# Performance work log

Measured on AMD Instinct MI355X. Metric: run time of the kernel, lower is better.

The kernel has to match this reference:

```python
import jax, jax.numpy as jnp
import numpy as np

B, L, H, N, DM = 16, 32768, 64, 16, 32


def setup_inputs() -> dict:
    key = jax.random.key(0)
    ks = jax.random.split(key, 16)
    inp = {}
    inp['x'] = jax.random.normal(ks[0], (B, L, H), dtype=jnp.float32)
    inp['control_parameters'] = jax.random.uniform(ks[1], (B, 2), dtype=jnp.float32)
    inp['W0'] = jax.random.normal(ks[2], (2, DM), dtype=jnp.float32) / np.sqrt(2.0)
    inp['b0'] = jnp.zeros((DM,), dtype=jnp.float32)
    inp['W1'] = jax.random.normal(ks[3], (DM, DM), dtype=jnp.float32) / np.sqrt(DM)
    inp['b1'] = jnp.zeros((DM,), dtype=jnp.float32)
    inp['W2'] = jax.random.normal(ks[4], (DM, DM), dtype=jnp.float32) / np.sqrt(DM)
    inp['b2'] = jnp.zeros((DM,), dtype=jnp.float32)
    # BlockV1 input linear
    inp['W_lin'] = jax.random.normal(ks[5], (H, H), dtype=jnp.float32) / np.sqrt(H)
    inp['b_lin'] = jnp.zeros((H,), dtype=jnp.float32)
    # DSSM / S4D parameters (S4D-Lin init)
    log_dt_min, log_dt_max = np.log(1e-3), np.log(1e-1)
    inp['log_dt'] = (log_dt_min + (log_dt_max - log_dt_min)
                     * jax.random.uniform(ks[6], (H,), dtype=jnp.float32))
    inp['A_re'] = -0.5 * jnp.ones((H, N), dtype=jnp.float32)
    inp['A_im'] = jnp.broadcast_to(np.pi * jnp.arange(N, dtype=jnp.float32), (H, N)).copy()
    inp['C_re'] = jax.random.normal(ks[7], (H, N), dtype=jnp.float32) / np.sqrt(2.0)
    inp['C_im'] = jax.random.normal(ks[8], (H, N), dtype=jnp.float32) / np.sqrt(2.0)
    inp['D'] = jax.random.normal(ks[9], (H,), dtype=jnp.float32)
    # FiLM: Linear(DM, 2*H) -> (gamma, beta)
    inp['W_film'] = jax.random.normal(ks[10], (DM, 2 * H), dtype=jnp.float32) / np.sqrt(DM)
    inp['b_film'] = jnp.zeros((2 * H,), dtype=jnp.float32)
    return inp


def _s4d_kernel(log_dt, A_re, A_im, C_re, C_im, length):
    # Diagonal SSM (S4D) convolution kernel via ZOH discretization.
    dt = jnp.exp(log_dt)[:, None]                      # [H,1]
    A = A_re + 1j * A_im                               # [H,N]
    dtA = dt * A                                       # [H,N]
    C = (C_re + 1j * C_im) * (jnp.exp(dtA) - 1.0) / A  # [H,N]
    t = jnp.arange(length, dtype=jnp.float32)          # [L]
    # Vandermonde: K[h,l] = 2 * Re( sum_n C[h,n] * exp(dtA[h,n])^l )
    vand = jnp.exp(dtA[:, :, None] * t)                # [H,N,L] complex
    return 2.0 * jnp.einsum('hn,hnl->hl', C, vand).real


def reference(x, control_parameters, W0, b0, W1, b1, W2, b2,
              W_lin, b_lin, log_dt, A_re, A_im, C_re, C_im, D,
              W_film, b_film):
    gelu = jax.nn.gelu
    # control-parameter MLP -> conditioning vector [B, DM]
    cond = gelu(control_parameters @ W0 + b0)
    cond = gelu(cond @ W1 + b1)
    cond = gelu(cond @ W2 + b2)
    # BlockV1: Linear + act
    h = gelu(x @ W_lin + b_lin)          # [B,L,H]
    u = jnp.swapaxes(h, 1, 2)            # [B,H,L]
    length = u.shape[-1]
    # S4D global convolution via FFT (linear, non-circular)
    K = _s4d_kernel(log_dt, A_re, A_im, C_re, C_im, length)   # [H,L]
    n = 2 * length
    Kf = jnp.fft.rfft(K, n=n)            # [H, n//2+1]
    uf = jnp.fft.rfft(u, n=n)            # [B,H, n//2+1]
    y = jnp.fft.irfft(uf * Kf, n=n)[..., :length] + D[:, None] * u  # [B,H,L]
    y = jnp.swapaxes(y, 1, 2)            # [B,L,H]
    # FiLM conditioning (no batch norm)
    gb = cond @ W_film + b_film          # [B, 2H]
    g, b = jnp.split(gb, 2, axis=-1)     # [B,H] each
    y = gelu(y * g[:, None, :] + b[:, None, :])
    # side-chain gate: elementwise multiply with input
    return x * y
```

## Files before the change

kernel.cpp:

```cpp
#include <hip/hip_runtime.h>
#include <hip/hip_bf16.h>
#include <math.h>

#define B_ 16
#define L_ 32768
#define H_ 64
#define N_ 16
#define DM_ 32
#define T_ 128
#define C_ 256
#define TS_ 16
#define US_ 68

typedef __attribute__((ext_vector_type(8))) short short8;
typedef __attribute__((ext_vector_type(4))) float floatx4;
typedef __attribute__((ext_vector_type(2))) float f32x2;

__device__ __forceinline__ float fast_gelu(float v) {
    float z = fmaf(0.044715f * v, v * v, v) * 0.7978845608028654f;
#if __has_builtin(__builtin_amdgcn_exp2f) && __has_builtin(__builtin_amdgcn_rcpf)
    float e = __builtin_amdgcn_exp2f(z * 2.8853900817779268f);
    float t = 1.0f - 2.0f * __builtin_amdgcn_rcpf(e + 1.0f);
#else
    float t = tanhf(z);
#endif
    return 0.5f * v * (1.0f + t);
}

__device__ __forceinline__ unsigned short bf16_rne(float f) {
    unsigned u = __float_as_uint(f);
    return (unsigned short)((u + 0x7FFFu + ((u >> 16) & 1u)) >> 16);
}
__device__ __forceinline__ float bf16_tof(unsigned short h) {
    return __uint_as_float(((unsigned)h) << 16);
}
__device__ __forceinline__ void cvt8(const float* f, short8* hi, short8* lo) {
    union { unsigned u[4]; short8 s; } Hh, Ll;
    #pragma unroll
    for (int jp = 0; jp < 4; ++jp) {
        unsigned short h0 = bf16_rne(f[2*jp]), h1 = bf16_rne(f[2*jp+1]);
        Hh.u[jp] = (unsigned)h0 | ((unsigned)h1 << 16);
        float l0 = f[2*jp]   - bf16_tof(h0);
        float l1 = f[2*jp+1] - bf16_tof(h1);
        Ll.u[jp] = (unsigned)bf16_rne(l0) | ((unsigned)bf16_rne(l1) << 16);
    }
    *hi = Hh.s; *lo = Ll.s;
}

__device__ __forceinline__ void pk_step(f32x2& s, f32x2 w, f32x2 uv0) {
    f32x2 t;
    asm("v_pk_fma_f32 %0, %1, %2, %3 op_sel:[1,1,0] op_sel_hi:[1,0,1] neg_lo:[1,0,0]"
        : "=v"(t) : "v"(w), "v"(s), "v"(uv0));
    asm("v_pk_fma_f32 %0, %1, %0, %2 op_sel_hi:[0,1,1]"
        : "+v"(s) : "v"(w), "v"(t));
}
__device__ __forceinline__ void pk_acc(f32x2& y, f32x2 c, f32x2 s) {
    asm("v_pk_fma_f32 %0, %1, %2, %0"
        : "+v"(y) : "v"(c), "v"(s));
}

__global__ void cond_film_kernel(const float* __restrict__ cp,
    const float* __restrict__ W0, const float* __restrict__ b0,
    const float* __restrict__ W1, const float* __restrict__ b1,
    const float* __restrict__ W2, const float* __restrict__ b2,
    const float* __restrict__ Wf, const float* __restrict__ bf,
    float* __restrict__ film) {
    __shared__ float ca[B_][DM_];
    __shared__ float cb[B_][DM_];
    int tid = threadIdx.x;
    int b = tid >> 5, j = tid & 31;
    float acc = fmaf(cp[b*2+0], W0[j], fmaf(cp[b*2+1], W0[DM_+j], b0[j]));
    ca[b][j] = fast_gelu(acc);
    __syncthreads();
    acc = b1[j];
    #pragma unroll
    for (int i = 0; i < DM_; ++i) acc = fmaf(ca[b][i], W1[i*DM_+j], acc);
    cb[b][j] = fast_gelu(acc);
    __syncthreads();
    acc = b2[j];
    #pragma unroll
    for (int i = 0; i < DM_; ++i) acc = fmaf(cb[b][i], W2[i*DM_+j], acc);
    float c2 = fast_gelu(acc);
    __syncthreads();
    ca[b][j] = c2;
    __syncthreads();
    #pragma unroll
    for (int t = 0; t < 4; ++t) {
        int k = j + DM_*t;
        float a = bf[k];
        #pragma unroll
        for (int i = 0; i < DM_; ++i) a = fmaf(ca[b][i], Wf[i*2*H_+k], a);
        film[b*2*H_ + k] = a;
    }
}

__global__ void coef_kernel(const float* __restrict__ log_dt,
    const float* __restrict__ A_re, const float* __restrict__ A_im,
    const float* __restrict__ C_re, const float* __restrict__ C_im,
    float* __restrict__ coef) {
    int g = blockIdx.x * blockDim.x + threadIdx.x;
    if (g >= H_*N_) return;
    int h = g >> 4, n = g & 15;
    float dt = expf(log_dt[h]);
    float Ar = A_re[h*N_+n], Ai = A_im[h*N_+n];
    float ar = dt*Ar, ai = dt*Ai;
    float er = expf(ar);
    float wr = er * cosf(ai), wi = er * sinf(ai);
    float eT = expf((float)T_ * ar);
    float aT = (float)T_ * ai;
    float wTr = eT * cosf(aT), wTi = eT * sinf(aT);
    float d  = Ar*Ar + Ai*Ai;
    float nr = wr - 1.0f, ni = wi;
    float qr = (nr*Ar + ni*Ai) / d;
    float qi = (ni*Ar - nr*Ai) / d;
    float Cr = C_re[h*N_+n], Ci = C_im[h*N_+n];
    float cr = 2.0f * (Cr*qr - Ci*qi);
    float ci = 2.0f * (Cr*qi + Ci*qr);
    coef[(n*6+0)*H_+h] = wr;
    coef[(n*6+1)*H_+h] = wi;
    coef[(n*6+2)*H_+h] = wTr;
    coef[(n*6+3)*H_+h] = wTi;
    coef[(n*6+4)*H_+h] = cr;
    coef[(n*6+5)*H_+h] = ci;
}

__global__ void chunk_scan_kernel(float* __restrict__ states,
                                  const float* __restrict__ coef) {
    int t = blockIdx.x * blockDim.x + threadIdx.x;
    int h = t & 63, n = (t >> 6) & 15, b = t >> 10;
    float wTr = coef[(n*6+2)*H_+h], wTi = coef[(n*6+3)*H_+h];
    float2* sp = (float2*)states + ((size_t)b*C_)*N_*H_ + (size_t)n*H_ + h;
    const int stride = N_*H_;
    float car = 0.f, cai = 0.f;
    float2 buf[8];
    #pragma unroll
    for (int i = 0; i < 8; ++i) buf[i] = sp[(size_t)i*stride];
    for (int cg = 0; cg < C_; cg += 8) {
        float2 nb[8];
        #pragma unroll
        for (int i = 0; i < 8; ++i)
            nb[i] = (cg + 8 + i < C_) ? sp[(size_t)(cg+8+i)*stride]
                                      : make_float2(0.f, 0.f);
        #pragma unroll
        for (int i = 0; i < 8; ++i) {
            float2 v = buf[i];
            sp[(size_t)(cg+i)*stride] = make_float2(car, cai);
            float nr2 = fmaf(wTr, car, fmaf(-wTi, cai, v.x));
            float ni2 = fmaf(wTr, cai, fmaf( wTi, car, v.y));
            car = nr2; cai = ni2;
            buf[i] = nb[i];
        }
    }
}

template<int PHASE>
__global__ __launch_bounds__(256, 3)
void gemm_scan_kernel(const float* __restrict__ x,
                      const float* __restrict__ W_lin, const float* __restrict__ b_lin,
                      const float* __restrict__ coef, float* __restrict__ states,
                      const float* __restrict__ D, const float* __restrict__ film,
                      float* __restrict__ out) {
    __shared__ __align__(16) unsigned short Wf[16*64*8];
    __shared__ float uld[4][TS_*US_];
    const int lane = threadIdx.x & 63;
    const int wv   = threadIdx.x >> 6;
    const int q    = blockIdx.x*4 + wv;
    const int b    = q >> 8;
    const int c    = q & 255;
    const int m    = lane & 15;
    const int quad = lane >> 4;

    for (int kt = 0; kt < 2; ++kt)
        for (int nt = 0; nt < 4; ++nt) {
            float f[8];
            #pragma unroll
            for (int j = 0; j < 8; ++j)
                f[j] = W_lin[(kt*32 + quad*8 + j)*H_ + nt*16 + m];
            short8 hi, lo;
            cvt8(f, &hi, &lo);
            ((short8*)Wf)[(kt*4 + nt)*64 + lane]     = hi;
            ((short8*)Wf)[((2+kt)*4 + nt)*64 + lane] = lo;
        }

    f32x2 w2[N_], s2[N_], c2[N_];
    float g_ = 0.f, be_ = 0.f, Dh = 0.f;
    #pragma unroll
    for (int n = 0; n < N_; ++n) {
        w2[n].x = coef[(n*6+0)*H_ + lane];
        w2[n].y = coef[(n*6+1)*H_ + lane];
    }
    if (PHASE == 1) {
        #pragma unroll
        for (int n = 0; n < N_; ++n) s2[n] = (f32x2){0.f, 0.f};
    } else {
        #pragma unroll
        for (int n = 0; n < N_; ++n) {
            c2[n].x = coef[(n*6+4)*H_ + lane];
            c2[n].y = coef[(n*6+5)*H_ + lane];
            size_t idx = (((size_t)q*N_ + n)*H_ + lane)*2;
            s2[n] = *(const f32x2*)(states + idx);
        }
        g_  = film[b*2*H_ + lane];
        be_ = film[b*2*H_ + H_ + lane];
        Dh  = D[lane];
    }
    float blv[4];
    #pragma unroll
    for (int nt = 0; nt < 4; ++nt) blv[nt] = b_lin[nt*16 + m];

    const float* xp = x + ((size_t)b*L_ + (size_t)c*T_)*H_;
    float* op = out + ((size_t)b*L_ + (size_t)c*T_)*H_;
    float* myu = uld[wv];

    for (int s = 0; s < T_/TS_; ++s) {
        const float* xs = xp + s*TS_*H_;
        short8 ah[2], al[2];
        #pragma unroll
        for (int kt = 0; kt < 2; ++kt) {
            const float* src = xs + m*H_ + kt*32 + quad*8;
            float4 v0 = *(const float4*)(src);
            float4 v1 = *(const float4*)(src + 4);
            float f[8] = {v0.x, v0.y, v0.z, v0.w, v1.x, v1.y, v1.z, v1.w};
            cvt8(f, &ah[kt], &al[kt]);
        }
        #pragma unroll
        for (int nt = 0; nt < 4; ++nt) {
            floatx4 acc = {0.f, 0.f, 0.f, 0.f};
            #pragma unroll
            for (int kt = 0; kt < 2; ++kt) {
                short8 bh = ((short8*)Wf)[(kt*4 + nt)*64 + lane];
                short8 bl = ((short8*)Wf)[((2+kt)*4 + nt)*64 + lane];
                acc = __builtin_amdgcn_mfma_f32_16x16x32_bf16(ah[kt], bh, acc, 0, 0, 0);
                acc = __builtin_amdgcn_mfma_f32_16x16x32_bf16(al[kt], bh, acc, 0, 0, 0);
                acc = __builtin_amdgcn_mfma_f32_16x16x32_bf16(ah[kt], bl, acc, 0, 0, 0);
            }
            #pragma unroll
            for (int r = 0; r < 4; ++r) {
                int row = quad*4 + r;
                float uv = fast_gelu(acc[r] + blv[nt]);
                myu[row*US_ + nt*16 + m] = uv;
            }
        }
        for (int l = 0; l < TS_; ++l) {
            float uv = myu[l*US_ + lane];
            f32x2 uv0 = {uv, 0.f};
            if (PHASE == 1) {
                #pragma unroll
                for (int n = 0; n < N_; ++n) pk_step(s2[n], w2[n], uv0);
            } else {
                float xg = xs[l*H_ + lane];
                f32x2 y2 = {0.f, 0.f};
                #pragma unroll
                for (int n = 0; n < N_; ++n) {
                    pk_step(s2[n], w2[n], uv0);
                    pk_acc(y2, c2[n], s2[n]);
                }
                float y  = fmaf(Dh, uv, y2.x - y2.y);
                float yg = fast_gelu(fmaf(y, g_, be_));
                op[(s*TS_ + l)*H_ + lane] = xg * yg;
            }
        }
    }
    if (PHASE == 1) {
        #pragma unroll
        for (int n = 0; n < N_; ++n) {
            size_t idx = (((size_t)q*N_ + n)*H_ + lane)*2;
            *(f32x2*)(states + idx) = s2[n];
        }
    }
}

extern "C" void kernel_launch(void* const* d_in, const int* in_sizes, int n_in,
                              void* d_out, int out_size, void* d_ws, size_t ws_size,
                              hipStream_t stream) {
    const float* x     = (const float*)d_in[0];
    const float* cp    = (const float*)d_in[1];
    const float* W0    = (const float*)d_in[2];
    const float* b0    = (const float*)d_in[3];
    const float* W1    = (const float*)d_in[4];
    const float* b1    = (const float*)d_in[5];
    const float* W2    = (const float*)d_in[6];
    const float* b2    = (const float*)d_in[7];
    const float* W_lin = (const float*)d_in[8];
    const float* b_lin = (const float*)d_in[9];
    const float* log_dt= (const float*)d_in[10];
    const float* A_re  = (const float*)d_in[11];
    const float* A_im  = (const float*)d_in[12];
    const float* C_re  = (const float*)d_in[13];
    const float* C_im  = (const float*)d_in[14];
    const float* D     = (const float*)d_in[15];
    const float* W_f   = (const float*)d_in[16];
    const float* b_f   = (const float*)d_in[17];
    float* out = (float*)d_out;

    float* film   = (float*)d_ws;
    float* coef   = film + B_*2*H_;
    float* states = coef + 6*H_*N_;

    cond_film_kernel<<<1, 512, 0, stream>>>(cp, W0, b0, W1, b1, W2, b2,
                                            W_f, b_f, film);
    coef_kernel<<<4, 256, 0, stream>>>(log_dt, A_re, A_im, C_re, C_im, coef);
    gemm_scan_kernel<1><<<(B_*C_)/4, 256, 0, stream>>>(x, W_lin, b_lin, coef,
                                                       states, nullptr, nullptr, nullptr);
    chunk_scan_kernel<<<(B_*N_*H_)/256, 256, 0, stream>>>(states, coef);
    gemm_scan_kernel<3><<<(B_*C_)/4, 256, 0, stream>>>(x, W_lin, b_lin, coef,
                                                       states, D, film, out);
}
```

Measured before the change: 502.6 us.

## Double chunk count to 512 and stage x tile in LDS for output phase

Halves the chunk length (128 to 64 steps) so twice as many wavefronts run the two scan phases, shortening each wave's serial recurrence. The chunk-scan and coef kernels are parameterized accordingly, with a fallback to the old 256-chunk config if the workspace is too small. In phase 3, the x tile is copied into shared memory while loading for the GEMM, so the gate multiply reads LDS instead of re-reading global memory. The per-step u and x values are also prefetched one step ahead. The trade-offs are a doubled state buffer, a longer sequential inter-chunk scan, and extra LDS usage that may lower occupancy.

```diff
diff --git a/kernel.cpp b/kernel.cpp
--- a/kernel.cpp
+++ b/kernel.cpp
@@ -7,8 +7,6 @@
 #define H_ 64
 #define N_ 16
 #define DM_ 32
-#define T_ 128
-#define C_ 256
 #define TS_ 16
 #define US_ 68
 
@@ -97,7 +95,7 @@
 __global__ void coef_kernel(const float* __restrict__ log_dt,
     const float* __restrict__ A_re, const float* __restrict__ A_im,
     const float* __restrict__ C_re, const float* __restrict__ C_im,
-    float* __restrict__ coef) {
+    float* __restrict__ coef, float Tf) {
     int g = blockIdx.x * blockDim.x + threadIdx.x;
     if (g >= H_*N_) return;
     int h = g >> 4, n = g & 15;
@@ -106,8 +104,8 @@
     float ar = dt*Ar, ai = dt*Ai;
     float er = expf(ar);
     float wr = er * cosf(ai), wi = er * sinf(ai);
-    float eT = expf((float)T_ * ar);
-    float aT = (float)T_ * ai;
+    float eT = expf(Tf * ar);
+    float aT = Tf * ai;
     float wTr = eT * cosf(aT), wTi = eT * sinf(aT);
     float d  = Ar*Ar + Ai*Ai;
     float nr = wr - 1.0f, ni = wi;
@@ -125,21 +123,21 @@
 }
 
 __global__ void chunk_scan_kernel(float* __restrict__ states,
-                                  const float* __restrict__ coef) {
+                                  const float* __restrict__ coef, int Cc) {
     int t = blockIdx.x * blockDim.x + threadIdx.x;
     int h = t & 63, n = (t >> 6) & 15, b = t >> 10;
     float wTr = coef[(n*6+2)*H_+h], wTi = coef[(n*6+3)*H_+h];
-    float2* sp = (float2*)states + ((size_t)b*C_)*N_*H_ + (size_t)n*H_ + h;
+    float2* sp = (float2*)states + ((size_t)b*Cc)*N_*H_ + (size_t)n*H_ + h;
     const int stride = N_*H_;
     float car = 0.f, cai = 0.f;
     float2 buf[8];
     #pragma unroll
     for (int i = 0; i < 8; ++i) buf[i] = sp[(size_t)i*stride];
-    for (int cg = 0; cg < C_; cg += 8) {
+    for (int cg = 0; cg < Cc; cg += 8) {
         float2 nb[8];
         #pragma unroll
         for (int i = 0; i < 8; ++i)
-            nb[i] = (cg + 8 + i < C_) ? sp[(size_t)(cg+8+i)*stride]
+            nb[i] = (cg + 8 + i < Cc) ? sp[(size_t)(cg+8+i)*stride]
                                       : make_float2(0.f, 0.f);
         #pragma unroll
         for (int i = 0; i < 8; ++i) {
@@ -153,20 +151,22 @@
     }
 }
 
-template<int PHASE>
+template<int PHASE, int CC>
 __global__ __launch_bounds__(256, 3)
 void gemm_scan_kernel(const float* __restrict__ x,
                       const float* __restrict__ W_lin, const float* __restrict__ b_lin,
                       const float* __restrict__ coef, float* __restrict__ states,
                       const float* __restrict__ D, const float* __restrict__ film,
                       float* __restrict__ out) {
+    constexpr int TT = L_/CC;
     __shared__ __align__(16) unsigned short Wf[16*64*8];
     __shared__ float uld[4][TS_*US_];
+    __shared__ float xld[(PHASE==3) ? 4*TS_*US_ : 4];
     const int lane = threadIdx.x & 63;
     const int wv   = threadIdx.x >> 6;
     const int q    = blockIdx.x*4 + wv;
-    const int b    = q >> 8;
-    const int c    = q & 255;
+    const int b    = q / CC;
+    const int c    = q % CC;
     const int m    = lane & 15;
     const int quad = lane >> 4;
 
@@ -208,11 +208,12 @@
     #pragma unroll
     for (int nt = 0; nt < 4; ++nt) blv[nt] = b_lin[nt*16 + m];
 
-    const float* xp = x + ((size_t)b*L_ + (size_t)c*T_)*H_;
-    float* op = out + ((size_t)b*L_ + (size_t)c*T_)*H_;
+    const float* xp = x + ((size_t)b*L_ + (size_t)c*TT)*H_;
+    float* op = out + ((size_t)b*L_ + (size_t)c*TT)*H_;
     float* myu = uld[wv];
-
-    for (int s = 0; s < T_/TS_; ++s) {
+    float* myx = (PHASE==3) ? &xld[wv*TS_*US_] : nullptr;
+
+    for (int s = 0; s < TT/TS_; ++s) {
         const float* xs = xp + s*TS_*H_;
         short8 ah[2], al[2];
         #pragma unroll
@@ -220,6 +221,11 @@
             const float* src = xs + m*H_ + kt*32 + quad*8;
             float4 v0 = *(const float4*)(src);
             float4 v1 = *(const float4*)(src + 4);
+            if (PHASE == 3) {
+                float* dst = &myx[m*US_ + kt*32 + quad*8];
+                *(float4*)(dst)     = v0;
+                *(float4*)(dst + 4) = v1;
+            }
             float f[8] = {v0.x, v0.y, v0.z, v0.w, v1.x, v1.y, v1.z, v1.w};
             cvt8(f, &ah[kt], &al[kt]);
         }
@@ -241,24 +247,28 @@
                 myu[row*US_ + nt*16 + m] = uv;
             }
         }
+        float uvc = myu[lane];
+        float xgc = (PHASE==3) ? myx[lane] : 0.f;
         for (int l = 0; l < TS_; ++l) {
-            float uv = myu[l*US_ + lane];
-            f32x2 uv0 = {uv, 0.f};
+            int ln = (l+1) & (TS_-1);
+            float uvn = myu[ln*US_ + lane];
+            float xgn = (PHASE==3) ? myx[ln*US_ + lane] : 0.f;
+            f32x2 uv0 = {uvc, 0.f};
             if (PHASE == 1) {
                 #pragma unroll
                 for (int n = 0; n < N_; ++n) pk_step(s2[n], w2[n], uv0);
             } else {
-                float xg = xs[l*H_ + lane];
                 f32x2 y2 = {0.f, 0.f};
                 #pragma unroll
                 for (int n = 0; n < N_; ++n) {
                     pk_step(s2[n], w2[n], uv0);
                     pk_acc(y2, c2[n], s2[n]);
                 }
-                float y  = fmaf(Dh, uv, y2.x - y2.y);
+                float y  = fmaf(Dh, uvc, y2.x - y2.y);
                 float yg = fast_gelu(fmaf(y, g_, be_));
-                op[(s*TS_ + l)*H_ + lane] = xg * yg;
+                op[(s*TS_ + l)*H_ + lane] = xgc * yg;
             }
+            uvc = uvn; xgc = xgn;
         }
     }
     if (PHASE == 1) {
@@ -299,10 +309,24 @@
 
     cond_film_kernel<<<1, 512, 0, stream>>>(cp, W0, b0, W1, b1, W2, b2,
                                             W_f, b_f, film);
-    coef_kernel<<<4, 256, 0, stream>>>(log_dt, A_re, A_im, C_re, C_im, coef);
-    gemm_scan_kernel<1><<<(B_*C_)/4, 256, 0, stream>>>(x, W_lin, b_lin, coef,
-                                                       states, nullptr, nullptr, nullptr);
-    chunk_scan_kernel<<<(B_*N_*H_)/256, 256, 0, stream>>>(states, coef);
-    gemm_scan_kernel<3><<<(B_*C_)/4, 256, 0, stream>>>(x, W_lin, b_lin, coef,
-                                                       states, D, film, out);
-}
+
+    size_t need64 = (size_t)(B_*2*H_ + 6*H_*N_)*4
+                  + (size_t)B_*512*N_*H_*2*4;
+    if (ws_size >= need64) {
+        coef_kernel<<<4, 256, 0, stream>>>(log_dt, A_re, A_im, C_re, C_im,
+                                           coef, 64.0f);
+        gemm_scan_kernel<1,512><<<(B_*512)/4, 256, 0, stream>>>(
+            x, W_lin, b_lin, coef, states, nullptr, nullptr, nullptr);
+        chunk_scan_kernel<<<(B_*N_*H_)/256, 256, 0, stream>>>(states, coef, 512);
+        gemm_scan_kernel<3,512><<<(B_*512)/4, 256, 0, stream>>>(
+            x, W_lin, b_lin, coef, states, D, film, out);
+    } else {
+        coef_kernel<<<4, 256, 0, stream>>>(log_dt, A_re, A_im, C_re, C_im,
+                                           coef, 128.0f);
+        gemm_scan_kernel<1,256><<<(B_*256)/4, 256, 0, stream>>>(
+            x, W_lin, b_lin, coef, states, nullptr, nullptr, nullptr);
+        chunk_scan_kernel<<<(B_*N_*H_)/256, 256, 0, stream>>>(states, coef, 256);
+        gemm_scan_kernel<3,256><<<(B_*256)/4, 256, 0, stream>>>(
+            x, W_lin, b_lin, coef, states, D, film, out);
+    }
+}
```

After: 500.6 us. Within noise of the previous version (-0.4%).
